# Optimization experiments

Measured on AMD Instinct MI355X. Metric: run time of the kernel, lower is better.

Reference implementation:

```python
import jax, jax.numpy as jnp
import numpy as np

B, C, D = 8192, 1000, 128
ALPHA = 0.5      # margin scale
LAMBDA = 0.5     # likelihood-margin weight
LAM2 = 0.1       # SCL weight
T = 0.3          # SCL temperature


def l2_normalized(x):
    # matches F.normalize(p=2, dim=1) with eps clamp
    n = jnp.maximum(jnp.linalg.norm(x, axis=1, keepdims=True), 1e-12)
    return x / n


def scl_loss(feat, labels, t):
    # vectorized form of the original O(B^2) python double loop
    sim = jnp.matmul(feat, feat.T) / t                     # [B, B]
    eye = jnp.eye(feat.shape[0], dtype=bool)
    exp_sim = jnp.where(eye, 0.0, jnp.exp(sim))
    bottom = exp_sim.sum(axis=1)                            # [B] denominator over k != i
    log_ratio = sim - jnp.log(bottom)[:, None]              # log(exp(sim_ij)/bottom_i)
    pos = (labels[:, None] == labels[None, :]) & (~eye)     # same-label pairs, j != i
    cnt = pos.sum(axis=1)
    sum_log = jnp.where(pos, log_ratio, 0.0).sum(axis=1)
    valid = cnt > 0
    per_i = jnp.where(valid, sum_log / jnp.maximum(cnt, 1), 0.0)
    n_sample = valid.sum()
    return -per_i.sum() / jnp.maximum(n_sample, 1)


def setup_inputs() -> dict:
    key = jax.random.key(0)
    k1, k2, k3 = jax.random.split(key, 3)
    feat = jax.random.normal(k1, (B, D), dtype=jnp.float32)
    labels = jax.random.randint(k2, (B,), 0, C, dtype=jnp.int64)
    # xavier_uniform_ with gain sqrt(2): bound = gain * sqrt(6/(fan_in+fan_out))
    bound = np.sqrt(2.0) * np.sqrt(6.0 / (C + D))
    means = jax.random.uniform(k3, (C, D), dtype=jnp.float32, minval=-bound, maxval=bound)
    return {"feat": feat, "labels": labels, "means": means}


def reference(feat, labels, means):
    feat_n = l2_normalized(feat)                            # scl=True path
    # neg squared distance to (unnormalized) means
    XY = jnp.matmul(feat_n, means.T)                        # [B, C]
    XX = (feat_n ** 2).sum(axis=1, keepdims=True)           # [B, 1]
    YY = (means ** 2).sum(axis=1)[None, :]                  # [1, C]
    neg_sqr_dist = -0.5 * (XX - 2.0 * XY + YY)

    # margin logits: multiply true-class logit by (1 + alpha)
    K = 1.0 + ALPHA * jax.nn.one_hot(labels, C, dtype=neg_sqr_dist.dtype)
    logits = neg_sqr_dist * K
    log_p = jax.nn.log_softmax(logits, axis=1)
    ce = -log_p[jnp.arange(B), labels].mean()

    means_n = l2_normalized(means)                          # scl=True normalizes means too
    means_batch = means_n[labels]                           # [B, D]
    loss_margin = ((feat_n - means_batch) ** 2).sum() / 2.0 / B

    scl = scl_loss(feat_n, labels, T)
    loss = (1.0 - LAM2) * ce + LAM2 * scl + LAMBDA * loss_margin
    return neg_sqr_dist, loss
```

## Files before the change

### kernel.cpp

```cpp
#include <hip/hip_runtime.h>
#include <math.h>

#define BN 8192
#define CN 1000
#define DN 128
#define INVT (1.0f/0.3f)
#define EXP2C 4.80898346962988f
#define NEGBIG (-1e30f)

typedef __bf16 bf16x8 __attribute__((ext_vector_type(8)));
typedef float  f32x4  __attribute__((ext_vector_type(4)));

#define F_FEATN  0
#define F_MEANSN 1048576
#define F_XX     1176576
#define F_YY     1184768
#define F_DIAG   1185768
#define F_FEATB  1193960
#define F_MEANSB 1718248
#define F_PL     1808360
#define F_BOT    1939432
#define F_CNT    1947624
#define F_CSUM   1948624
#define F_RED    2076624

#define NB_SCL  544
#define NB_NSD  512
#define NB_CSUM 512

__device__ __forceinline__ void async16(const void* g, void* s) {
    __builtin_amdgcn_global_load_lds(
        (const __attribute__((address_space(1))) void*)g,
        (__attribute__((address_space(3))) void*)s, 16, 0, 0);
}

__global__ void norm_feat(const float* __restrict__ src, float* __restrict__ dst,
                          float* __restrict__ sq, __bf16* __restrict__ dstb,
                          float* __restrict__ diag, const int* __restrict__ labels,
                          int* __restrict__ counts) {
    int row = blockIdx.x * 4 + (threadIdx.x >> 6);
    int lane = threadIdx.x & 63;
    float f0 = src[row * DN + lane];
    float f1 = src[row * DN + 64 + lane];
    float ss = f0 * f0 + f1 * f1;
    #pragma unroll
    for (int o = 32; o > 0; o >>= 1) ss += __shfl_xor(ss, o);
    float inv = 1.0f / fmaxf(sqrtf(ss), 1e-12f);
    float n0 = f0 * inv, n1 = f1 * inv;
    dst[row * DN + lane] = n0;
    dst[row * DN + 64 + lane] = n1;
    __bf16 b0 = (__bf16)n0, b1 = (__bf16)n1;
    dstb[row * DN + lane] = b0;
    dstb[row * DN + 64 + lane] = b1;
    float fb0 = (float)b0, fb1 = (float)b1;
    float sb = fb0 * fb0 + fb1 * fb1;
    #pragma unroll
    for (int o = 32; o > 0; o >>= 1) sb += __shfl_xor(sb, o);
    if (lane == 0) {
        diag[row] = sb;
        sq[row] = ss * inv * inv;
        atomicAdd(&counts[labels[row]], 1);
    }
}

__global__ void norm_means(const float* __restrict__ src, float* __restrict__ dst,
                           float* __restrict__ sq, __bf16* __restrict__ dstb) {
    int row = blockIdx.x * 4 + (threadIdx.x >> 6);
    int lane = threadIdx.x & 63;
    float f0 = (row < CN) ? src[row * DN + lane] : 0.f;
    float f1 = (row < CN) ? src[row * DN + 64 + lane] : 0.f;
    dstb[row * DN + lane] = (__bf16)f0;
    dstb[row * DN + 64 + lane] = (__bf16)f1;
    if (row >= CN) return;
    float ss = f0 * f0 + f1 * f1;
    #pragma unroll
    for (int o = 32; o > 0; o >>= 1) ss += __shfl_xor(ss, o);
    float inv = 1.0f / fmaxf(sqrtf(ss), 1e-12f);
    dst[row * DN + lane] = f0 * inv;
    dst[row * DN + 64 + lane] = f1 * inv;
    if (lane == 0) sq[row] = ss;
}

__device__ __forceinline__ void stage128(uint4* sT, const uint4* __restrict__ src,
                                         int row0, int tid) {
    #pragma unroll
    for (int s = 0; s < 8; s++) {
        int c = tid + s * 256;
        int r = c >> 4, ch = c & 15;
        sT[r * 16 + (ch ^ (r & 7))] = src[(size_t)(row0 + r) * 16 + ch];
    }
}

__global__ __launch_bounds__(256, 2) void mega_kernel(
        const __bf16* __restrict__ featb, const __bf16* __restrict__ meansb,
        const float* __restrict__ featn, const int* __restrict__ labels,
        const float* __restrict__ xx, const float* __restrict__ yy,
        float* __restrict__ out, float* __restrict__ pl,
        float* __restrict__ bottom, float* __restrict__ csum) {
    __shared__ uint4 sh[2][2048];
    int bx = blockIdx.x;
    int tid = threadIdx.x;
    int lane = tid & 63, w = tid >> 6;
    int q = lane >> 4, l15 = lane & 15;

    if (bx < NB_SCL) {
        int rem = bx, I = 0;
        while (true) { int ns = (64 - I + 3) >> 2; if (rem < ns) break; rem -= ns; ++I; }
        int J0 = I + rem * 4;
        int len = min(4, 64 - J0);
        int i0 = I * 128;
        const uint4* fv = (const uint4*)featb;
        int wrow = (w >> 1) * 64, wcol = (w & 1) * 64;

        bf16x8 af[4][4];
        #pragma unroll
        for (int ii = 0; ii < 4; ii++) {
            size_t r = (size_t)(i0 + wrow + ii * 16 + l15) * 16;
            #pragma unroll
            for (int kk = 0; kk < 4; kk++)
                af[ii][kk] = *(const bf16x8*)&fv[r + kk * 4 + q];
        }
        float bs[4][4] = {};

        auto stage = [&](int row0, int buf) {
            #pragma unroll
            for (int s = 0; s < 8; s++) {
                int rb = w * 32 + s * 4;
                int r = rb + q;
                async16(&fv[(size_t)(row0 + r) * 16 + (l15 ^ (r & 7))], &sh[buf][rb * 16]);
            }
        };

        stage(J0 * 128, 0);
        if (len > 1) stage(J0 * 128 + 128, 1);

        for (int t = 0; t < len; t++) {
            if (t + 1 < len) asm volatile("s_waitcnt vmcnt(8)" ::: "memory");
            else             asm volatile("s_waitcnt vmcnt(0)" ::: "memory");
            __builtin_amdgcn_s_barrier();
            const uint4* B = sh[t & 1];

            f32x4 acc[4][4];
            #pragma unroll
            for (int ii = 0; ii < 4; ii++)
                #pragma unroll
                for (int jj = 0; jj < 4; jj++) acc[ii][jj] = (f32x4){0.f, 0.f, 0.f, 0.f};
            #pragma unroll
            for (int kk = 0; kk < 4; kk++) {
                bf16x8 bfv[4];
                #pragma unroll
                for (int jj = 0; jj < 4; jj++) {
                    int r = wcol + jj * 16 + l15;
                    bfv[jj] = *(const bf16x8*)&B[r * 16 + ((kk * 4 + q) ^ (r & 7))];
                }
                #pragma unroll
                for (int ii = 0; ii < 4; ii++)
                    #pragma unroll
                    for (int jj = 0; jj < 4; jj++)
                        acc[ii][jj] = __builtin_amdgcn_mfma_f32_16x16x32_bf16(
                            af[ii][kk], bfv[jj], acc[ii][jj], 0, 0, 0);
            }

            int jt = (J0 + t) * 128;
            float cp[4] = {0.f, 0.f, 0.f, 0.f};
            #pragma unroll
            for (int ii = 0; ii < 4; ii++)
                #pragma unroll
                for (int jj = 0; jj < 4; jj++)
                    #pragma unroll
                    for (int r4 = 0; r4 < 4; r4++) {
                        float e = exp2f(acc[ii][jj][r4] * EXP2C);
                        bs[ii][r4] += e;
                        cp[jj] += e;
                    }
            if (J0 + t != I) {
                #pragma unroll
                for (int jj = 0; jj < 4; jj++) {
                    float c = cp[jj];
                    c += __shfl_xor(c, 16);
                    c += __shfl_xor(c, 32);
                    if (lane < 16)
                        atomicAdd(&bottom[jt + wcol + jj * 16 + l15], c);
                }
            }
            __builtin_amdgcn_s_barrier();
            if (t + 2 < len) stage((J0 + t + 2) * 128, t & 1);
        }

        int ibase = i0 + wrow + q * 4;
        #pragma unroll
        for (int ii = 0; ii < 4; ii++)
            #pragma unroll
            for (int r4 = 0; r4 < 4; r4++) {
                float b = bs[ii][r4];
                #pragma unroll
                for (int o = 8; o > 0; o >>= 1) b += __shfl_xor(b, o);
                if (l15 == 0) atomicAdd(&bottom[ibase + ii * 16 + r4], b);
            }

    } else if (bx < NB_SCL + NB_NSD) {
        int b = bx - NB_SCL;
        int i0 = (b >> 3) * 128, j0 = (b & 7) * 128;
        stage128(sh[0], (const uint4*)featb, i0, tid);
        stage128(sh[1], (const uint4*)meansb, j0, tid);
        __syncthreads();
        int wrow = (w >> 1) * 64, wcol = (w & 1) * 64;
        int ibase = i0 + wrow + q * 4;

        f32x4 acc[4][4];
        #pragma unroll
        for (int ii = 0; ii < 4; ii++)
            #pragma unroll
            for (int jj = 0; jj < 4; jj++) acc[ii][jj] = (f32x4){0.f, 0.f, 0.f, 0.f};
        #pragma unroll
        for (int kk = 0; kk < 4; kk++) {
            bf16x8 af[4], bfv[4];
            #pragma unroll
            for (int ii = 0; ii < 4; ii++) {
                int r = wrow + ii * 16 + l15;
                af[ii] = *(const bf16x8*)&sh[0][r * 16 + ((kk * 4 + q) ^ (r & 7))];
            }
            #pragma unroll
            for (int jj = 0; jj < 4; jj++) {
                int r = wcol + jj * 16 + l15;
                bfv[jj] = *(const bf16x8*)&sh[1][r * 16 + ((kk * 4 + q) ^ (r & 7))];
            }
            #pragma unroll
            for (int ii = 0; ii < 4; ii++)
                #pragma unroll
                for (int jj = 0; jj < 4; jj++)
                    acc[ii][jj] = __builtin_amdgcn_mfma_f32_16x16x32_bf16(
                        af[ii], bfv[jj], acc[ii][jj], 0, 0, 0);
        }
        int jg[4]; float yv[4];
        #pragma unroll
        for (int jj = 0; jj < 4; jj++) {
            jg[jj] = j0 + wcol + jj * 16 + l15;
            yv[jj] = (jg[jj] < CN) ? yy[jg[jj]] : 0.f;
        }
        int pslot = ((b & 7) * 2 + (w & 1)) * BN;
        #pragma unroll
        for (int ii = 0; ii < 4; ii++) {
            int rbase = ibase + ii * 16;
            float4 xv = ((const float4*)xx)[rbase >> 2];
            int4 lv = ((const int4*)labels)[rbase >> 2];
            float xa[4] = {xv.x, xv.y, xv.z, xv.w};
            int la[4] = {lv.x, lv.y, lv.z, lv.w};
            #pragma unroll
            for (int r4 = 0; r4 < 4; r4++) {
                int ig = rbase + r4;
                float s = 0.f;
                #pragma unroll
                for (int jj = 0; jj < 4; jj++) {
                    float v = -0.5f * (xa[r4] - 2.f * acc[ii][jj][r4] + yv[jj]);
                    bool ok = (jg[jj] < CN);
                    if (ok) out[(size_t)ig * CN + jg[jj]] = v;
                    float l = (jg[jj] == la[r4]) ? 1.5f * v : v;
                    s += ok ? __expf(l) : 0.f;
                }
                #pragma unroll
                for (int o = 8; o > 0; o >>= 1) s += __shfl_xor(s, o);
                if (l15 == 0) pl[pslot + ig] = s;
            }
        }

    } else {
        int b2 = bx - NB_SCL - NB_NSD;
        for (int idx = b2 * 256 + tid; idx < BN * DN; idx += NB_CSUM * 256) {
            int row = idx >> 7, d = idx & 127;
            atomicAdd(&csum[labels[row] * DN + d], featn[idx]);
        }
    }
}

__global__ void cemp_kernel(const float* __restrict__ featn, const float* __restrict__ meansn,
        const float* __restrict__ csum, const int* __restrict__ labels,
        const float* __restrict__ pl, const float* __restrict__ out,
        const float* __restrict__ bottom, const int* __restrict__ counts,
        const float* __restrict__ diag, const float* __restrict__ xx,
        float* __restrict__ red) {
    int tid = threadIdx.x;
    int lane = tid & 63, w = tid >> 6;
    float a_sp = 0.f, a_nv = 0.f, a_ce = 0.f, a_mg = 0.f;
    for (int pass = 0; pass < 4; pass++) {
        int row = blockIdx.x * 16 + pass * 4 + w;
        int lab = labels[row];
        float f0 = featn[row * DN + lane],  f1 = featn[row * DN + 64 + lane];
        float m0 = meansn[lab * DN + lane], m1 = meansn[lab * DN + 64 + lane];
        float c0 = csum[lab * DN + lane],   c1 = csum[lab * DN + 64 + lane];
        float d0 = f0 - m0, d1 = f1 - m1;
        float ss = d0 * d0 + d1 * d1;
        float pp = f0 * c0 + f1 * c1;
        #pragma unroll
        for (int o = 32; o > 0; o >>= 1) {
            ss += __shfl_xor(ss, o);
            pp += __shfl_xor(pp, o);
        }
        if (lane == 0) {
            float S = 0.f;
            #pragma unroll
            for (int k = 0; k < 16; k++) S += pl[k * BN + row];
            a_ce += logf(S) - 1.5f * out[(size_t)row * CN + lab];
            a_mg += ss;
            float bot = bottom[row] - __expf(diag[row] * INVT);
            float pv = (pp - xx[row]) * INVT;
            int c = counts[lab] - 1;
            if (c > 0) {
                a_sp += pv / (float)c - logf(bot);
                a_nv += 1.f;
            }
        }
    }
    __shared__ float r4[4][4];
    if (lane == 0) { r4[w][0] = a_sp; r4[w][1] = a_nv; r4[w][2] = a_ce; r4[w][3] = a_mg; }
    __syncthreads();
    if (tid < 4)
        atomicAdd(&red[tid], r4[0][tid] + r4[1][tid] + r4[2][tid] + r4[3][tid]);
}

__global__ void final_fin(const float* __restrict__ red, float* __restrict__ loss_out) {
    float SP = red[0], NV = red[1], CE = red[2], MG = red[3];
    float scl = -SP / fmaxf(NV, 1.f);
    loss_out[0] = 0.9f * (CE / (float)BN) + 0.1f * scl + 0.5f * (MG / (2.f * (float)BN));
}

extern "C" void kernel_launch(void* const* d_in, const int* in_sizes, int n_in,
                              void* d_out, int out_size, void* d_ws, size_t ws_size,
                              hipStream_t stream) {
    const float* feat   = (const float*)d_in[0];
    const int*   labels = (const int*)d_in[1];
    const float* means  = (const float*)d_in[2];
    float* out = (float*)d_out;
    float* ws  = (float*)d_ws;

    float*  featn  = ws + F_FEATN;
    float*  meansn = ws + F_MEANSN;
    float*  xx     = ws + F_XX;
    float*  yy     = ws + F_YY;
    float*  diag   = ws + F_DIAG;
    __bf16* featb  = (__bf16*)(ws + F_FEATB);
    __bf16* meansb = (__bf16*)(ws + F_MEANSB);
    float*  pl     = ws + F_PL;
    float*  bottom = ws + F_BOT;
    int*    counts = (int*)(ws + F_CNT);
    float*  csum   = ws + F_CSUM;
    float*  red    = ws + F_RED;

    hipMemsetAsync(ws + F_BOT, 0, (size_t)(8192 + 1000 + 128000 + 4) * sizeof(float), stream);

    norm_feat<<<2048, 256, 0, stream>>>(feat, featn, xx, featb, diag, labels, counts);
    norm_means<<<256, 256, 0, stream>>>(means, meansn, yy, meansb);
    mega_kernel<<<NB_SCL + NB_NSD + NB_CSUM, 256, 0, stream>>>(
        featb, meansb, featn, labels, xx, yy, out, pl, bottom, csum);
    cemp_kernel<<<512, 256, 0, stream>>>(featn, meansn, csum, labels, pl, out,
                                         bottom, counts, diag, xx, red);
    final_fin<<<1, 1, 0, stream>>>(red, out + (size_t)BN * CN);
}
```

Baseline: 128.7 us.

## Shrink per-block tiles to 64 rows, single LDS buffer, raise occupancy

Both the SCL and distance sections of the fused kernel now use 64-row A tiles instead of 128, which doubles the block counts and halves the per-wave accumulators. The SCL blocks loop over up to 8 column tiles. LDS drops to one 32KB buffer and the launch bound rises to 3 blocks per SM, with the aim of more occupancy and better load balance. The cost is that the double-buffered async prefetch is gone, so each SCL tile now waits on a synchronous stage between two barriers, and the B tiles are re-read from global memory twice as often.

Result: faster. 125.6 us (-2.4%).

```diff
diff --git a/kernel.cpp b/kernel.cpp
--- a/kernel.cpp
+++ b/kernel.cpp
@@ -6,7 +6,6 @@
 #define DN 128
 #define INVT (1.0f/0.3f)
 #define EXP2C 4.80898346962988f
-#define NEGBIG (-1e30f)
 
 typedef __bf16 bf16x8 __attribute__((ext_vector_type(8)));
 typedef float  f32x4  __attribute__((ext_vector_type(4)));
@@ -24,8 +23,8 @@
 #define F_CSUM   1948624
 #define F_RED    2076624
 
-#define NB_SCL  544
-#define NB_NSD  512
+#define NB_SCL  576
+#define NB_NSD  1024
 #define NB_CSUM 512
 
 __device__ __forceinline__ void async16(const void* g, void* s) {
@@ -81,68 +80,57 @@
     if (lane == 0) sq[row] = ss;
 }
 
-__device__ __forceinline__ void stage128(uint4* sT, const uint4* __restrict__ src,
-                                         int row0, int tid) {
-    #pragma unroll
-    for (int s = 0; s < 8; s++) {
-        int c = tid + s * 256;
-        int r = c >> 4, ch = c & 15;
-        sT[r * 16 + (ch ^ (r & 7))] = src[(size_t)(row0 + r) * 16 + ch];
-    }
-}
-
-__global__ __launch_bounds__(256, 2) void mega_kernel(
+__global__ __launch_bounds__(256, 3) void mega_kernel(
         const __bf16* __restrict__ featb, const __bf16* __restrict__ meansb,
         const float* __restrict__ featn, const int* __restrict__ labels,
         const float* __restrict__ xx, const float* __restrict__ yy,
         float* __restrict__ out, float* __restrict__ pl,
         float* __restrict__ bottom, float* __restrict__ csum) {
-    __shared__ uint4 sh[2][2048];
+    __shared__ uint4 sh[2048];
     int bx = blockIdx.x;
     int tid = threadIdx.x;
     int lane = tid & 63, w = tid >> 6;
     int q = lane >> 4, l15 = lane & 15;
+    int wrow = (w >> 1) * 32, wcol = (w & 1) * 64;
+
+    auto stageA = [&](const uint4* src, int row0) {
+        #pragma unroll
+        for (int s = 0; s < 8; s++) {
+            int rb = w * 32 + s * 4;
+            int r = rb + q;
+            async16(&src[(size_t)(row0 + r) * 16 + (l15 ^ (r & 7))], &sh[rb * 16]);
+        }
+    };
 
     if (bx < NB_SCL) {
-        int rem = bx, I = 0;
-        while (true) { int ns = (64 - I + 3) >> 2; if (rem < ns) break; rem -= ns; ++I; }
-        int J0 = I + rem * 4;
-        int len = min(4, 64 - J0);
-        int i0 = I * 128;
+        int rem = bx, a = 0;
+        while (true) { int ns = (64 - (a >> 1) + 7) >> 3; if (rem < ns) break; rem -= ns; ++a; }
+        int A = a >> 1;
+        int J0 = A + rem * 8;
+        int len = min(8, 64 - J0);
+        int i0 = a * 64;
         const uint4* fv = (const uint4*)featb;
-        int wrow = (w >> 1) * 64, wcol = (w & 1) * 64;
-
-        bf16x8 af[4][4];
-        #pragma unroll
-        for (int ii = 0; ii < 4; ii++) {
+
+        bf16x8 af[2][4];
+        #pragma unroll
+        for (int ii = 0; ii < 2; ii++) {
             size_t r = (size_t)(i0 + wrow + ii * 16 + l15) * 16;
             #pragma unroll
             for (int kk = 0; kk < 4; kk++)
                 af[ii][kk] = *(const bf16x8*)&fv[r + kk * 4 + q];
         }
-        float bs[4][4] = {};
-
-        auto stage = [&](int row0, int buf) {
-            #pragma unroll
-            for (int s = 0; s < 8; s++) {
-                int rb = w * 32 + s * 4;
-                int r = rb + q;
-                async16(&fv[(size_t)(row0 + r) * 16 + (l15 ^ (r & 7))], &sh[buf][rb * 16]);
-            }
-        };
-
-        stage(J0 * 128, 0);
-        if (len > 1) stage(J0 * 128 + 128, 1);
+        float bs[2][4] = {};
 
         for (int t = 0; t < len; t++) {
-            if (t + 1 < len) asm volatile("s_waitcnt vmcnt(8)" ::: "memory");
-            else             asm volatile("s_waitcnt vmcnt(0)" ::: "memory");
-            __builtin_amdgcn_s_barrier();
-            const uint4* B = sh[t & 1];
-
-            f32x4 acc[4][4];
-            #pragma unroll
-            for (int ii = 0; ii < 4; ii++)
+            int J = J0 + t;
+            int j0 = J * 128;
+            __syncthreads();
+            stageA(fv, j0);
+            __syncthreads();
+
+            f32x4 acc[2][4];
+            #pragma unroll
+            for (int ii = 0; ii < 2; ii++)
                 #pragma unroll
                 for (int jj = 0; jj < 4; jj++) acc[ii][jj] = (f32x4){0.f, 0.f, 0.f, 0.f};
             #pragma unroll
@@ -151,20 +139,19 @@
                 #pragma unroll
                 for (int jj = 0; jj < 4; jj++) {
                     int r = wcol + jj * 16 + l15;
-                    bfv[jj] = *(const bf16x8*)&B[r * 16 + ((kk * 4 + q) ^ (r & 7))];
+                    bfv[jj] = *(const bf16x8*)&sh[r * 16 + ((kk * 4 + q) ^ (r & 7))];
                 }
                 #pragma unroll
-                for (int ii = 0; ii < 4; ii++)
+                for (int ii = 0; ii < 2; ii++)
                     #pragma unroll
                     for (int jj = 0; jj < 4; jj++)
                         acc[ii][jj] = __builtin_amdgcn_mfma_f32_16x16x32_bf16(
                             af[ii][kk], bfv[jj], acc[ii][jj], 0, 0, 0);
             }
 
-            int jt = (J0 + t) * 128;
             float cp[4] = {0.f, 0.f, 0.f, 0.f};
             #pragma unroll
-            for (int ii = 0; ii < 4; ii++)
+            for (int ii = 0; ii < 2; ii++)
                 #pragma unroll
                 for (int jj = 0; jj < 4; jj++)
                     #pragma unroll
@@ -173,23 +160,20 @@
                         bs[ii][r4] += e;
                         cp[jj] += e;
                     }
-            if (J0 + t != I) {
+            if (J != A) {
                 #pragma unroll
                 for (int jj = 0; jj < 4; jj++) {
                     float c = cp[jj];
                     c += __shfl_xor(c, 16);
                     c += __shfl_xor(c, 32);
                     if (lane < 16)
-                        atomicAdd(&bottom[jt + wcol + jj * 16 + l15], c);
+                        atomicAdd(&bottom[j0 + wcol + jj * 16 + l15], c);
                 }
             }
-            __builtin_amdgcn_s_barrier();
-            if (t + 2 < len) stage((J0 + t + 2) * 128, t & 1);
-        }
-
+        }
         int ibase = i0 + wrow + q * 4;
         #pragma unroll
-        for (int ii = 0; ii < 4; ii++)
+        for (int ii = 0; ii < 2; ii++)
             #pragma unroll
             for (int r4 = 0; r4 < 4; r4++) {
                 float b = bs[ii][r4];
@@ -200,37 +184,39 @@
 
     } else if (bx < NB_SCL + NB_NSD) {
         int b = bx - NB_SCL;
-        int i0 = (b >> 3) * 128, j0 = (b & 7) * 128;
-        stage128(sh[0], (const uint4*)featb, i0, tid);
-        stage128(sh[1], (const uint4*)meansb, j0, tid);
+        int i0 = (b >> 3) * 64, j0 = (b & 7) * 128;
+        const uint4* fv = (const uint4*)featb;
+        stageA((const uint4*)meansb, j0);
+
+        bf16x8 af[2][4];
+        #pragma unroll
+        for (int ii = 0; ii < 2; ii++) {
+            size_t r = (size_t)(i0 + wrow + ii * 16 + l15) * 16;
+            #pragma unroll
+            for (int kk = 0; kk < 4; kk++)
+                af[ii][kk] = *(const bf16x8*)&fv[r + kk * 4 + q];
+        }
         __syncthreads();
-        int wrow = (w >> 1) * 64, wcol = (w & 1) * 64;
-        int ibase = i0 + wrow + q * 4;
-
-        f32x4 acc[4][4];
-        #pragma unroll
-        for (int ii = 0; ii < 4; ii++)
+
+        f32x4 acc[2][4];
+        #pragma unroll
+        for (int ii = 0; ii < 2; ii++)
             #pragma unroll
             for (int jj = 0; jj < 4; jj++) acc[ii][jj] = (f32x4){0.f, 0.f, 0.f, 0.f};
         #pragma unroll
         for (int kk = 0; kk < 4; kk++) {
-            bf16x8 af[4], bfv[4];
-            #pragma unroll
-            for (int ii = 0; ii < 4; ii++) {
-                int r = wrow + ii * 16 + l15;
-                af[ii] = *(const bf16x8*)&sh[0][r * 16 + ((kk * 4 + q) ^ (r & 7))];
-            }
+            bf16x8 bfv[4];
             #pragma unroll
             for (int jj = 0; jj < 4; jj++) {
                 int r = wcol + jj * 16 + l15;
-                bfv[jj] = *(const bf16x8*)&sh[1][r * 16 + ((kk * 4 + q) ^ (r & 7))];
-            }
-            #pragma unroll
-            for (int ii = 0; ii < 4; ii++)
+                bfv[jj] = *(const bf16x8*)&sh[r * 16 + ((kk * 4 + q) ^ (r & 7))];
+            }
+            #pragma unroll
+            for (int ii = 0; ii < 2; ii++)
                 #pragma unroll
                 for (int jj = 0; jj < 4; jj++)
                     acc[ii][jj] = __builtin_amdgcn_mfma_f32_16x16x32_bf16(
-                        af[ii], bfv[jj], acc[ii][jj], 0, 0, 0);
+                        af[ii][kk], bfv[jj], acc[ii][jj], 0, 0, 0);
         }
         int jg[4]; float yv[4];
         #pragma unroll
@@ -239,8 +225,9 @@
             yv[jj] = (jg[jj] < CN) ? yy[jg[jj]] : 0.f;
         }
         int pslot = ((b & 7) * 2 + (w & 1)) * BN;
-        #pragma unroll
-        for (int ii = 0; ii < 4; ii++) {
+        int ibase = i0 + wrow + q * 4;
+        #pragma unroll
+        for (int ii = 0; ii < 2; ii++) {
             int rbase = ibase + ii * 16;
             float4 xv = ((const float4*)xx)[rbase >> 2];
             int4 lv = ((const int4*)labels)[rbase >> 2];
```
